# Performance work log

Measured on AMD Instinct MI355X. Metric: run time of the kernel, lower is better.

Reference implementation:

```python
import jax, jax.numpy as jnp
import numpy as np
import math

B, S, H, NH = 1, 2048, 1024, 16  # batch, seq, hidden, heads


def setup_inputs() -> dict:
    key = jax.random.key(0)
    ks = jax.random.split(key, 12)
    inp = {
        "query": jax.random.normal(ks[0], (B, S, H), dtype=jnp.float32),
        "key": jax.random.normal(ks[1], (B, S, H), dtype=jnp.float32),
        "value": jax.random.normal(ks[2], (B, S, H), dtype=jnp.float32),
        "attention_mask": jax.random.randint(ks[3], (1, 1, S, S), 0, 2, dtype=jnp.int32),
        # torch nn.Linear params: y = x @ W.T + b, W init ~ U(-1/sqrt(H), 1/sqrt(H))
        "Wq": jax.random.uniform(ks[4], (H, H), jnp.float32, -1, 1) / math.sqrt(H),
        "bq": jax.random.uniform(ks[5], (H,), jnp.float32, -1, 1) / math.sqrt(H),
        "Wk": jax.random.uniform(ks[6], (H, H), jnp.float32, -1, 1) / math.sqrt(H),
        "bk": jax.random.uniform(ks[7], (H,), jnp.float32, -1, 1) / math.sqrt(H),
        "Wv": jax.random.uniform(ks[8], (H, H), jnp.float32, -1, 1) / math.sqrt(H),
        "bv": jax.random.uniform(ks[9], (H,), jnp.float32, -1, 1) / math.sqrt(H),
        "Wo": jax.random.uniform(ks[10], (H, H), jnp.float32, -1, 1) / math.sqrt(H),
        "bo": jax.random.uniform(ks[11], (H,), jnp.float32, -1, 1) / math.sqrt(H),
        "head": NH,
        "hidden_size": H,
    }
    return inp


def reference(query, key, value, attention_mask, Wq, bq, Wk, bk, Wv, bv, Wo, bo, head, hidden_size):
    b, s, _ = query.shape
    d_k = hidden_size // head

    def proj(x, W, bias):
        # [b, s, hidden] -> [b, head, s, d_k]
        y = x @ W.T + bias
        return y.reshape(b, s, head, d_k).transpose(0, 2, 1, 3)

    q = proj(query, Wq, bq)
    k = proj(key, Wk, bk)
    v = proj(value, Wv, bv)

    # naive full score matrix, as in the source (scale by sqrt(d_k) = last dim of q)
    scores = jnp.einsum("bhqd,bhkd->bhqk", q, k) / math.sqrt(d_k)
    # faithful quirk: masked positions are set to 0 (not -inf) before softmax
    scores = jnp.where(attention_mask == 0, jnp.zeros((), scores.dtype), scores)
    attn = jax.nn.softmax(scores, axis=-1)

    out = jnp.einsum("bhqk,bhkd->bhqd", attn, v)  # [b, head, s, d_k]
    out = out.transpose(0, 2, 1, 3).reshape(b, s, head * d_k)
    return out @ Wo.T + bo
```

## Files before the change

kernel.cpp:

```cpp
#include <hip/hip_runtime.h>
#include <hip/hip_bf16.h>


#define S_LEN 2048
#define HID   1024
#define NHEAD 16
#define DK    64

typedef unsigned short u16;
typedef __attribute__((ext_vector_type(8))) short bf16x8;
typedef __attribute__((ext_vector_type(4))) short bf16x4;
typedef __attribute__((ext_vector_type(4))) float f32x4;
typedef __attribute__((ext_vector_type(2))) unsigned u32x2;
typedef __attribute__((ext_vector_type(4))) unsigned u32x4;

__device__ __forceinline__ void load16_lds(const void* g, void* l) {
  __builtin_amdgcn_global_load_lds(
      (const __attribute__((address_space(1))) void*)g,
      (__attribute__((address_space(3))) void*)l, 16, 0, 0);
}

__device__ __forceinline__ short bfbits(float x) {
  __hip_bfloat16 h = __float2bfloat16(x);
  return *(short*)&h;
}
__device__ __forceinline__ bf16x8 cvt8(float4 a, float4 b) {
  bf16x8 r;
  r[0] = bfbits(a.x); r[1] = bfbits(a.y); r[2] = bfbits(a.z); r[3] = bfbits(a.w);
  r[4] = bfbits(b.x); r[5] = bfbits(b.y); r[6] = bfbits(b.z); r[7] = bfbits(b.w);
  return r;
}
__device__ __forceinline__ float bf2f(u16 u) {
  unsigned v = (unsigned)u << 16;
  return *(float*)&v;
}

__global__ __launch_bounds__(256) void cvt_pack_kernel(
    const float* __restrict__ q, const float* __restrict__ k,
    const float* __restrict__ v, const float* __restrict__ wq,
    const float* __restrict__ wk, const float* __restrict__ wv,
    const float* __restrict__ wo, const int* __restrict__ mask,
    u16* __restrict__ Xbf, u16* __restrict__ Wbf,
    unsigned int* __restrict__ bits) {
  const int y = blockIdx.y;
  if (y == 7) {
    if (blockIdx.x >= 512) return;
    int idx = blockIdx.x * 256 + threadIdx.x;
    const int4* p = (const int4*)(mask + (size_t)idx * 32);
    unsigned word = 0;
#pragma unroll
    for (int i = 0; i < 8; ++i) {
      int4 mv = p[i];
      word |= (unsigned)(mv.x != 0) << (i * 4 + 0);
      word |= (unsigned)(mv.y != 0) << (i * 4 + 1);
      word |= (unsigned)(mv.z != 0) << (i * 4 + 2);
      word |= (unsigned)(mv.w != 0) << (i * 4 + 3);
    }
    bits[idx] = word;
    return;
  }
  size_t i = ((size_t)blockIdx.x * 256 + threadIdx.x) * 8;
  const float* src;
  u16* dst;
  size_t n;
  if (y < 3) {
    src = y == 0 ? q : (y == 1 ? k : v);
    dst = Xbf + (size_t)y * (S_LEN * HID);
    n = (size_t)S_LEN * HID;
  } else {
    int w = y - 3;
    src = w == 0 ? wq : (w == 1 ? wk : (w == 2 ? wv : wo));
    dst = Wbf + (size_t)w * (HID * HID);
    n = (size_t)HID * HID;
  }
  if (i >= n) return;
  float4 a = *(const float4*)(src + i);
  float4 b = *(const float4*)(src + i + 4);
  *(bf16x8*)(dst + i) = cvt8(a, b);
}

__global__ __launch_bounds__(256, 3) void gemm_qkv(
    const u16* __restrict__ Xbf, const u16* __restrict__ Wbf,
    const float* __restrict__ bq, const float* __restrict__ bk,
    const float* __restrict__ bv, u16* __restrict__ Qb,
    u16* __restrict__ Kb, u16* __restrict__ Vt) {
  constexpr int Mm = 2048, Kk = 1024, NIT = 16;
  const int tid = threadIdx.x, lane = tid & 63, wave = tid >> 6;
  const int q4 = lane >> 4, c16 = lane & 15;
  const int bx = blockIdx.x;
  const int xcd = bx & 7, s = bx >> 3;
  const int mh = s / 24;
  const int mBase = ((xcd >> 1) * 4 + mh) * 128;
  const int nG = (xcd & 1) * 24 + (s - mh * 24);
  const int nBase = nG * 64;
  const int z = nBase >> 10;
  const u16* A = Xbf + (size_t)z * (S_LEN * HID);
  const float* bias = z == 0 ? bq : (z == 1 ? bk : bv);
  const float oscale = (z == 0) ? 0.125f * 1.44269504088896f : 1.0f;

  const int wr = wave >> 1, wc = wave & 1;

  __shared__ __align__(16) u16 As[2][2][128 * 32];
  __shared__ __align__(16) u16 Bs[2][2][64 * 32];

  f32x4 acc[4][2] = {};
  const int srow = lane >> 2;
  const int sx8 = ((lane & 3) ^ ((srow >> 1) & 3)) * 8;
  const int rx8 = (q4 ^ ((c16 >> 1) & 3)) * 8;

  auto issue = [&](int it, int buf) {
#pragma unroll
    for (int j = 0; j < 4; ++j) {
      int u = wave * 4 + j, h = u >> 3, grp = u & 7;
      load16_lds(A + (size_t)(mBase + grp * 16 + srow) * Kk + it * 64 +
                     h * 32 + sx8,
                 &As[buf][h][grp * 512]);
    }
#pragma unroll
    for (int j = 0; j < 2; ++j) {
      int u = wave * 2 + j, h = u >> 2, grp = u & 3;
      load16_lds(Wbf + (size_t)(nBase + grp * 16 + srow) * Kk + it * 64 +
                     h * 32 + sx8,
                 &Bs[buf][h][grp * 512]);
    }
  };

  issue(0, 0);
  __syncthreads();

  for (int it = 0; it < NIT; ++it) {
    const int buf = it & 1, nbuf = buf ^ 1;
    if (it + 1 < NIT) issue(it + 1, nbuf);
#pragma unroll
    for (int kk = 0; kk < 2; ++kk) {
      bf16x8 af[4], bfr[2];
#pragma unroll
      for (int t = 0; t < 4; ++t)
        af[t] = *(const bf16x8*)&As[buf][kk][(wr * 64 + t * 16 + c16) * 32 + rx8];
#pragma unroll
      for (int t = 0; t < 2; ++t)
        bfr[t] = *(const bf16x8*)&Bs[buf][kk][(wc * 32 + t * 16 + c16) * 32 + rx8];
#pragma unroll
      for (int mt = 0; mt < 4; ++mt)
#pragma unroll
        for (int nt = 0; nt < 2; ++nt)
          acc[mt][nt] = __builtin_amdgcn_mfma_f32_16x16x32_bf16(
              af[mt], bfr[nt], acc[mt][nt], 0, 0, 0);
    }
    __syncthreads();
  }

#pragma unroll
  for (int nt = 0; nt < 2; ++nt) {
    int colg = nBase + wc * 32 + nt * 16 + c16;
    int col = colg & 1023;
    float bv2 = bias[col];
#pragma unroll
    for (int mt = 0; mt < 4; ++mt) {
#pragma unroll
      for (int r = 0; r < 4; ++r) {
        int row = mBase + wr * 64 + mt * 16 + q4 * 4 + r;
        float v = (acc[mt][nt][r] + bv2) * oscale;
        if (z == 2) {
          int vv = row & 31;
          int rowp = (row & ~31) | (((vv & 15) >> 2) << 3) |
                     (((vv >> 4) & 1) << 2) | (vv & 3);
          ((__hip_bfloat16*)Vt)[(size_t)col * Mm + rowp] = __float2bfloat16(v);
        } else {
          u16* C = z == 0 ? Qb : Kb;
          ((__hip_bfloat16*)C)[(size_t)row * 1024 + col] = __float2bfloat16(v);
        }
      }
    }
  }
}

__global__ __launch_bounds__(512, 4) void attn_kernel(
    const u16* __restrict__ Qb, const u16* __restrict__ Kb,
    const u16* __restrict__ Vt, const unsigned* __restrict__ mb,
    u16* __restrict__ partOA, u16* __restrict__ partO3,
    float* __restrict__ partL) {
  constexpr int NITA = 8;
  const int lin = blockIdx.x + 8 * (blockIdx.y + 16 * blockIdx.z);
  const int work = ((lin & 7) << 6) | (lin >> 3);
  const int qt = work & 7, h = (work >> 3) & 15, zz = work >> 7;
  const int tid = threadIdx.x, lane = tid & 63, wave = tid >> 6;
  const int q4 = lane >> 4, c16 = lane & 15;

  __shared__ __align__(16) u16 Ks[2][2][64 * 32];
  __shared__ __align__(16) u16 Vs[2][2][64 * 32];

  const int q0 = qt * 256 + wave * 32;

  bf16x8 qf[2][2];
#pragma unroll
  for (int m = 0; m < 2; ++m)
#pragma unroll
    for (int kk = 0; kk < 2; ++kk)
      qf[m][kk] = *(const bf16x8*)(Qb + (size_t)(q0 + m * 16 + c16) * HID +
                                   h * DK + kk * 32 + q4 * 8);

  f32x4 o[2][4] = {};
  float l_lane[2] = {0.0f, 0.0f};

  const int srow = lane >> 2;
  const int sx8 = ((lane & 3) ^ ((srow >> 1) & 3)) * 8;
  const int rx8 = (q4 ^ ((c16 >> 1) & 3)) * 8;
  const int kvbase = zz * (S_LEN / 4);

  auto issueKV = [&](int it, int buf) {
    const int kv0 = kvbase + it * 64;
#pragma unroll
    for (int j = 0; j < 2; ++j) {
      int i = wave * 2 + j;
      if (i < 8) {
        int half = i >> 2, grp = i & 3;
        load16_lds(Kb + (size_t)(kv0 + grp * 16 + srow) * HID + h * DK +
                       half * 32 + sx8,
                   &Ks[buf][half][grp * 512]);
      } else {
        int ii = i - 8;
        int half = ii >> 2, grp = ii & 3;
        load16_lds(Vt + (size_t)(h * DK + grp * 16 + srow) * S_LEN + kv0 +
                       half * 32 + sx8,
                   &Vs[buf][half][grp * 512]);
      }
    }
  };

  issueKV(0, 0);
  __syncthreads();

  for (int it = 0; it < NITA; ++it) {
    const int buf = it & 1, nbuf = buf ^ 1;
    if (it + 1 < NITA) issueKV(it + 1, nbuf);

    u32x2 mw[2];
#pragma unroll
    for (int m = 0; m < 2; ++m)
      mw[m] = *(const u32x2*)(mb + (size_t)(q0 + m * 16 + c16) * 64 +
                              (kvbase >> 5) + it * 2);

#pragma unroll
    for (int kk = 0; kk < 2; ++kk) {
      f32x4 sv[2][2];
      __builtin_amdgcn_s_setprio(1);
#pragma unroll
      for (int ntb = 0; ntb < 2; ++ntb) {
        const int nt = kk * 2 + ntb;
        const int rsw = (nt * 16 + c16) * 32 + rx8;
        bf16x8 kf0 = *(const bf16x8*)&Ks[buf][0][rsw];
        bf16x8 kf1 = *(const bf16x8*)&Ks[buf][1][rsw];
#pragma unroll
        for (int m = 0; m < 2; ++m) {
          f32x4 a = {};
          a = __builtin_amdgcn_mfma_f32_16x16x32_bf16(kf0, qf[m][0], a, 0, 0, 0);
          a = __builtin_amdgcn_mfma_f32_16x16x32_bf16(kf1, qf[m][1], a, 0, 0, 0);
          sv[m][ntb] = a;
        }
      }
      __builtin_amdgcn_s_setprio(0);

      bf16x8 pa[2];
#pragma unroll
      for (int m = 0; m < 2; ++m) {
        const unsigned word = kk ? mw[m][1] : mw[m][0];
        float p[8];
#pragma unroll
        for (int ntb = 0; ntb < 2; ++ntb)
#pragma unroll
          for (int r = 0; r < 4; ++r) {
            const int bit = ntb * 16 + q4 * 4 + r;
            float s = ((word >> bit) & 1u) ? sv[m][ntb][r] : 0.0f;
            float e;
            asm("v_exp_f32 %0, %1" : "=v"(e) : "v"(s));
            l_lane[m] += e;
            p[ntb * 4 + r] = e;
          }
        u32x4 pk;
#pragma unroll
        for (int j = 0; j < 4; ++j)
          asm("v_cvt_pk_bf16_f32 %0, %1, %2"
              : "=v"(pk[j]) : "v"(p[2 * j]), "v"(p[2 * j + 1]));
        pa[m] = *(bf16x8*)&pk;
      }

      __builtin_amdgcn_s_setprio(1);
#pragma unroll
      for (int ntv = 0; ntv < 4; ++ntv) {
        const int rsw = (ntv * 16 + c16) * 32 + rx8;
        bf16x8 vb = *(const bf16x8*)&Vs[buf][kk][rsw];
        o[0][ntv] = __builtin_amdgcn_mfma_f32_16x16x32_bf16(pa[0], vb, o[0][ntv], 0, 0, 0);
        o[1][ntv] = __builtin_amdgcn_mfma_f32_16x16x32_bf16(pa[1], vb, o[1][ntv], 0, 0, 0);
      }
      __builtin_amdgcn_s_setprio(0);
    }
    __syncthreads();
  }

  u16* pO = (zz < 3) ? (partOA + (size_t)zz * (S_LEN * HID)) : partO3;
#pragma unroll
  for (int m = 0; m < 2; ++m) {
    float s = l_lane[m];
    s += __shfl_xor(s, 16);
    s += __shfl_xor(s, 32);
    int qrow = q0 + m * 16 + c16;
    if (q4 == 0)
      partL[((size_t)zz * NHEAD + h) * S_LEN + qrow] = s;
#pragma unroll
    for (int r = 0; r < 4; ++r) {
      int row = q0 + m * 16 + q4 * 4 + r;
#pragma unroll
      for (int nt = 0; nt < 4; ++nt)
        ((__hip_bfloat16*)pO)[(size_t)row * HID + h * DK + nt * 16 + c16] =
            __float2bfloat16(o[m][nt][r]);
    }
  }
}

__global__ __launch_bounds__(256) void gemm_out(
    const u16* __restrict__ pOA, const u16* __restrict__ pO3,
    const float* __restrict__ partL, const u16* __restrict__ Wo,
    const float* __restrict__ bo, float* __restrict__ out) {
  constexpr int Nn = 1024, Kk = 1024, NIT = 16;
  constexpr size_t M2 = (size_t)S_LEN * HID;
  const int tid = threadIdx.x, lane = tid & 63, wave = tid >> 6;
  const int q4 = lane >> 4, c16 = lane & 15;
  const int bx = blockIdx.x;
  const int xcd = bx & 7, s = bx >> 3;
  const int mBase = (xcd * 8 + (s & 7)) * 32;
  const int nBase = (s >> 3) * 128;
  const int wn = wave * 32;

  __shared__ __align__(16) u16 As[2][2][32 * 32];
  __shared__ __align__(16) u16 Bs[2][2][128 * 32];
  __shared__ float linv[32][16];

  f32x4 acc[2][2] = {};
  const int srow = lane >> 2;
  const int sx8 = ((lane & 3) ^ ((srow >> 1) & 3)) * 8;
  const int rx8 = (q4 ^ ((c16 >> 1) & 3)) * 8;

  const int arow = tid >> 3, acu = tid & 7;
  const int ahalf = acu >> 2;
  const int aoff = arow * 32 + ((acu & 3) ^ ((arow >> 1) & 3)) * 8;

  auto issueB = [&](int it, int buf) {
#pragma unroll
    for (int j = 0; j < 4; ++j) {
      int u = wave * 4 + j, h = u >> 3, grp = u & 7;
      load16_lds(Wo + (size_t)(nBase + grp * 16 + srow) * Kk + it * 64 +
                     h * 32 + sx8,
                 &Bs[buf][h][grp * 512]);
    }
  };

  bf16x8 avA[4], avB[4];
  auto aloadTo = [&](bf16x8* dst, int it) {
    const u16* p = pOA + (size_t)(mBase + arow) * Kk + it * 64 + acu * 8;
    dst[0] = *(const bf16x8*)p;
    dst[1] = *(const bf16x8*)(p + M2);
    dst[2] = *(const bf16x8*)(p + 2 * M2);
    dst[3] = *(const bf16x8*)(pO3 + (size_t)(mBase + arow) * Kk + it * 64 + acu * 8);
  };
  auto awriteFrom = [&](const bf16x8* src, int it, int buf) {
    float inv = linv[arow][it];
    bf16x8 r;
#pragma unroll
    for (int j = 0; j < 8; ++j) {
      float v = (bf2f((u16)src[0][j]) + bf2f((u16)src[1][j]) +
                 bf2f((u16)src[2][j]) + bf2f((u16)src[3][j])) * inv;
      r[j] = bfbits(v);
    }
    *(bf16x8*)&As[buf][ahalf][aoff] = r;
  };

#pragma unroll
  for (int e = 0; e < 2; ++e) {
    int idx = tid * 2 + e, row = idx >> 4, hh = idx & 15;
    float l = 0.0f;
#pragma unroll
    for (int z = 0; z < 4; ++z)
      l += partL[(size_t)(z * NHEAD + hh) * S_LEN + mBase + row];
    linv[row][hh] = 1.0f / l;
  }
  aloadTo(avA, 0);
  issueB(0, 0);
  __syncthreads();
  awriteFrom(avA, 0, 0);
  aloadTo(avB, 1);
  __syncthreads();

  for (int it = 0; it < NIT; ++it) {
    const int buf = it & 1, nbuf = buf ^ 1;
    if (it + 1 < NIT) issueB(it + 1, nbuf);
    if (it + 2 < NIT) aloadTo((it & 1) ? avB : avA, it + 2);
#pragma unroll
    for (int kk = 0; kk < 2; ++kk) {
      bf16x8 af[2], bfr[2];
#pragma unroll
      for (int t = 0; t < 2; ++t)
        af[t] = *(const bf16x8*)&As[buf][kk][(t * 16 + c16) * 32 + rx8];
#pragma unroll
      for (int t = 0; t < 2; ++t)
        bfr[t] = *(const bf16x8*)&Bs[buf][kk][(wn + t * 16 + c16) * 32 + rx8];
#pragma unroll
      for (int mt = 0; mt < 2; ++mt)
#pragma unroll
        for (int nt = 0; nt < 2; ++nt)
          acc[mt][nt] = __builtin_amdgcn_mfma_f32_16x16x32_bf16(
              af[mt], bfr[nt], acc[mt][nt], 0, 0, 0);
    }
    if (it + 1 < NIT) awriteFrom((it & 1) ? avA : avB, it + 1, nbuf);
    __syncthreads();
  }

#pragma unroll
  for (int nt = 0; nt < 2; ++nt) {
    int col = nBase + wn + nt * 16 + c16;
    float bv = bo[col];
#pragma unroll
    for (int mt = 0; mt < 2; ++mt)
#pragma unroll
      for (int r = 0; r < 4; ++r) {
        int row = mBase + mt * 16 + q4 * 4 + r;
        out[(size_t)row * Nn + col] = acc[mt][nt][r] + bv;
      }
  }
}

extern "C" void kernel_launch(void* const* d_in, const int* in_sizes, int n_in,
                              void* d_out, int out_size, void* d_ws, size_t ws_size,
                              hipStream_t stream) {
  const float* q    = (const float*)d_in[0];
  const float* k    = (const float*)d_in[1];
  const float* v    = (const float*)d_in[2];
  const int*   mask = (const int*)d_in[3];
  const float* Wq = (const float*)d_in[4];
  const float* bq = (const float*)d_in[5];
  const float* Wk = (const float*)d_in[6];
  const float* bk = (const float*)d_in[7];
  const float* Wv = (const float*)d_in[8];
  const float* bv = (const float*)d_in[9];
  const float* Wo = (const float*)d_in[10];
  const float* bo = (const float*)d_in[11];

  const size_t M2 = (size_t)S_LEN * HID;
  const size_t W1 = (size_t)HID * HID;
  const size_t need = (4 * W1 + 3 * M2 + 3 * M2) * 2 +
                      (size_t)S_LEN * 64 * 4 + 2 * NHEAD * S_LEN * 4;
  if (ws_size < need) return;

  u16* Wbf = (u16*)d_ws;
  u16* Xbf = Wbf + 4 * W1;
  u16* Qb = Xbf + 3 * M2;
  u16* Kb = Qb + M2;
  u16* Vt = Kb + M2;
  unsigned* mbits = (unsigned*)(Vt + M2);
  u16* partOA = Xbf;
  u16* partO3 = Wbf;
  float* partL = (float*)(Wbf + 2 * W1);

  hipLaunchKernelGGL(cvt_pack_kernel, dim3(1024, 8), dim3(256), 0, stream,
                     q, k, v, Wq, Wk, Wv, Wo, mask, Xbf, Wbf, mbits);

  hipLaunchKernelGGL(gemm_qkv, dim3(768), dim3(256), 0, stream,
                     Xbf, Wbf, bq, bk, bv, Qb, Kb, Vt);

  hipLaunchKernelGGL(attn_kernel, dim3(S_LEN / 256, NHEAD, 4), dim3(512), 0,
                     stream, Qb, Kb, Vt, mbits, partOA, partO3, partL);

  hipLaunchKernelGGL(gemm_out, dim3(512), dim3(256), 0, stream,
                     partOA, partO3, partL, Wbf + 3 * W1, bo, (float*)d_out);
}
```

Baseline: 195.2 us.

## Permute W rows in QKV projection to vectorize output stores and stage V transpose through LDS

The W row load order is permuted so each lane's two N-tiles hold adjacent output columns. For Q and K this lets the epilogue pack two bf16 values into one 32-bit store instead of scalar 16-bit stores. For the transposed V output, results are first written into LDS (reusing the A tile buffer) and then copied out as coalesced 16-byte rows. This targets the scattered narrow global writes of the epilogue, at the cost of an extra barrier and LDS traffic for the V path.

```diff
diff --git a/kernel.cpp b/kernel.cpp
--- a/kernel.cpp
+++ b/kernel.cpp
@@ -119,7 +119,10 @@
 #pragma unroll
     for (int j = 0; j < 2; ++j) {
       int u = wave * 2 + j, h = u >> 2, grp = u & 3;
-      load16_lds(Wbf + (size_t)(nBase + grp * 16 + srow) * Kk + it * 64 +
+      int brow = grp * 16 + srow;
+      int b32 = brow & 31;
+      int bsrc = (brow & 32) | ((b32 & 15) * 2 + (b32 >> 4));
+      load16_lds(Wbf + (size_t)(nBase + bsrc) * Kk + it * 64 +
                      h * 32 + sx8,
                  &Bs[buf][h][grp * 512]);
     }
@@ -150,26 +153,47 @@
     __syncthreads();
   }
 
-#pragma unroll
-  for (int nt = 0; nt < 2; ++nt) {
-    int colg = nBase + wc * 32 + nt * 16 + c16;
-    int col = colg & 1023;
-    float bv2 = bias[col];
+  const int colE = wc * 32 + c16 * 2;
+  if (z == 2) {
+    u16* LT = (u16*)&As[0][0][0];
+#pragma unroll
+    for (int nt = 0; nt < 2; ++nt) {
+      int col = colE + nt;
+      float bv2 = bias[((nBase & 1023) + col)];
+#pragma unroll
+      for (int mt = 0; mt < 4; ++mt) {
+        int row0 = wr * 64 + mt * 16 + q4 * 4;
+        int vv0 = row0 & 31;
+        int rowp0 = (row0 & ~31) | (((vv0 & 15) >> 2) << 3) |
+                    (((vv0 >> 4) & 1) << 2);
+        bf16x4 t;
+#pragma unroll
+        for (int r = 0; r < 4; ++r) t[r] = bfbits(acc[mt][nt][r] + bv2);
+        *(bf16x4*)&LT[col * 132 + rowp0] = t;
+      }
+    }
+    __syncthreads();
+#pragma unroll
+    for (int rep = 0; rep < 4; ++rep) {
+      int u = rep * 256 + tid;
+      int col = u >> 4, seg = u & 15;
+      bf16x8 vvv = *(const bf16x8*)&LT[col * 132 + seg * 8];
+      *(bf16x8*)(Vt + (size_t)((nBase & 1023) + col) * Mm + mBase + seg * 8) = vvv;
+    }
+  } else {
+    u16* C = z == 0 ? Qb : Kb;
+    int colg = (nBase & 1023) + colE;
+    float2 b2 = *(const float2*)&bias[colg];
 #pragma unroll
     for (int mt = 0; mt < 4; ++mt) {
 #pragma unroll
       for (int r = 0; r < 4; ++r) {
         int row = mBase + wr * 64 + mt * 16 + q4 * 4 + r;
-        float v = (acc[mt][nt][r] + bv2) * oscale;
-        if (z == 2) {
-          int vv = row & 31;
-          int rowp = (row & ~31) | (((vv & 15) >> 2) << 3) |
-                     (((vv >> 4) & 1) << 2) | (vv & 3);
-          ((__hip_bfloat16*)Vt)[(size_t)col * Mm + rowp] = __float2bfloat16(v);
-        } else {
-          u16* C = z == 0 ? Qb : Kb;
-          ((__hip_bfloat16*)C)[(size_t)row * 1024 + col] = __float2bfloat16(v);
-        }
+        float v0 = (acc[mt][0][r] + b2.x) * oscale;
+        float v1 = (acc[mt][1][r] + b2.y) * oscale;
+        unsigned pk;
+        asm("v_cvt_pk_bf16_f32 %0, %1, %2" : "=v"(pk) : "v"(v0), "v"(v1));
+        *(unsigned*)&C[(size_t)row * 1024 + colg] = pk;
       }
     }
   }
```

Result: faster. 188.9 us (-3.2%).
